# Optimization experiments

Measured on AMD Instinct MI355X. Metric: run time of the kernel, lower is better.

## Reference

```python
import jax, jax.numpy as jnp
import numpy as np

N_NODES = 20000
N_EDGES = 320000
IN_DIM = 64
H = 8      # num_heads
D = 16     # h_dim (out_dim)
CLAMP = 5.0


def setup_inputs() -> dict:
    key = jax.random.key(0)
    ks = jax.random.split(key, 12)
    inp = {
        'x': jax.random.normal(ks[0], (N_NODES, IN_DIM), jnp.float32),
        'edge_attr': jax.random.normal(ks[1], (N_EDGES, IN_DIM), jnp.float32),
        'edge_index': jax.random.randint(ks[2], (2, N_EDGES), 0, N_NODES),
        'Qw': jax.random.normal(ks[3], (IN_DIM, H * D), jnp.float32) * 0.1,
        'Qb': jnp.zeros((H * D,), jnp.float32),
        'Kw': jax.random.normal(ks[4], (IN_DIM, H * D), jnp.float32) * 0.1,
        'Kb': jnp.zeros((H * D,), jnp.float32),
        'Ew': jax.random.normal(ks[5], (IN_DIM, H * D * 2), jnp.float32) * 0.1,
        'Eb': jnp.zeros((H * D * 2,), jnp.float32),
        'Vw': jax.random.normal(ks[6], (IN_DIM, H * D), jnp.float32) * 0.1,
        'Vb': jnp.zeros((H * D,), jnp.float32),
        'Aw': jax.random.normal(ks[7], (D, H, 1), jnp.float32) * 0.1,
        'VeRow': jax.random.normal(ks[8], (D, H, D), jnp.float32) * 0.1,
    }
    return inp


def reference(x, edge_attr, edge_index, Qw, Qb, Kw, Kb, Ew, Eb, Vw, Vb, Aw, VeRow):
    N = x.shape[0]
    Ne = edge_attr.shape[0]
    src, dst = edge_index[0], edge_index[1]

    # node/edge projections (torch Linear stored as [in, out])
    Q_h = (x @ Qw + Qb).reshape(N, H, D)
    K_h = (x @ Kw + Kb).reshape(N, H, D)
    V_h = (x @ Vw + Vb).reshape(N, H, D)
    E = (edge_attr @ Ew + Eb).reshape(Ne, H, 2 * D)
    Ex1, Ex2 = E[:, :, :D], E[:, :, D:]

    # edge-wise additive score with signed-sqrt edge term  [Ne, H, D]
    s2 = Ex1 * Ex2
    score = K_h[src] + Q_h[dst] + jnp.sqrt(jax.nn.relu(s2)) - jnp.sqrt(jax.nn.relu(-s2))
    e_t = score
    oE = score.reshape(Ne, H * D)

    # attention logits: contract with Aw, clamp  [Ne, H, 1]
    a = jnp.einsum('ehd,dhc->ehc', score, Aw)
    a = jnp.clip(a, -CLAMP, CLAMP)

    # segment softmax over destination nodes
    m = jax.ops.segment_max(a, dst, num_segments=N)
    ea = jnp.exp(a - m[dst])
    denom = jax.ops.segment_sum(ea, dst, num_segments=N)
    attn = ea / (denom[dst] + 1e-16)  # [Ne, H, 1]

    # message passing: scatter-add to destination nodes
    oV = jax.ops.segment_sum(V_h[src] * attn, dst, num_segments=N)      # [N, H, D]
    rowV = jax.ops.segment_sum(e_t * attn, dst, num_segments=N)          # [N, H, D]
    rowV = jnp.einsum('nhd,dhc->nhc', rowV, VeRow)
    n_out = (oV + rowV).reshape(N, H * D)
    return n_out, oE
```

## Files before the change

kernel.cpp:

```cpp
#include <hip/hip_runtime.h>

#define IN_DIM 64
#define H 8
#define D 16
#define HD 128
#define CLAMP_V 5.0f
#define NCHUNK 8

typedef __attribute__((ext_vector_type(8))) short bf16x8;
typedef __attribute__((ext_vector_type(4))) float f32x4;

__device__ inline unsigned short f2b(float f) {
    unsigned int u = __float_as_uint(f);
    u += 0x7FFFu + ((u >> 16) & 1u);
    return (unsigned short)(u >> 16);
}
__device__ inline float b2f(unsigned short h) {
    return __uint_as_float((unsigned int)h << 16);
}
__device__ inline void split2(float f, unsigned short& hi, unsigned short& lo) {
    hi = f2b(f);
    lo = f2b(f - b2f(hi));
}

__global__ void __launch_bounds__(128) qkv_kernel(
    const float* __restrict__ x,
    const float* __restrict__ Qw, const float* __restrict__ Qb,
    const float* __restrict__ Kw, const float* __restrict__ Kb,
    const float* __restrict__ Vw, const float* __restrict__ Vb,
    float* __restrict__ Q, float* __restrict__ K, float* __restrict__ V)
{
    const int n0 = blockIdx.x * NCHUNK;
    const int t = threadIdx.x;
    __shared__ float xs[NCHUNK][IN_DIM];
    for (int i = t; i < NCHUNK * IN_DIM; i += 128)
        xs[i >> 6][i & 63] = x[(size_t)n0 * IN_DIM + i];
    __syncthreads();

    const float qb = Qb[t], kb = Kb[t], vb = Vb[t];
    float aq[NCHUNK], ak[NCHUNK], av[NCHUNK];
#pragma unroll
    for (int c = 0; c < NCHUNK; ++c) { aq[c] = qb; ak[c] = kb; av[c] = vb; }

#pragma unroll 4
    for (int k = 0; k < IN_DIM; ++k) {
        const float wq = Qw[k * HD + t];
        const float wk = Kw[k * HD + t];
        const float wv = Vw[k * HD + t];
#pragma unroll
        for (int c = 0; c < NCHUNK; ++c) {
            const float xv = xs[c][k];
            aq[c] = fmaf(xv, wq, aq[c]);
            ak[c] = fmaf(xv, wk, ak[c]);
            av[c] = fmaf(xv, wv, av[c]);
        }
    }
#pragma unroll
    for (int c = 0; c < NCHUNK; ++c) {
        Q[(size_t)(n0 + c) * HD + t] = aq[c];
        K[(size_t)(n0 + c) * HD + t] = ak[c];
        V[(size_t)(n0 + c) * HD + t] = av[c];
    }
}

__global__ void prep_ewt_kernel(const float* __restrict__ Ew, unsigned short* __restrict__ EwT)
{
    const int idx = blockIdx.x * 256 + threadIdx.x;
    const int k = idx >> 8, c = idx & 255;
    const float w = Ew[idx];
    unsigned short hi, lo;
    split2(w, hi, lo);
    EwT[c * 64 + k] = hi;
    EwT[16384 + c * 64 + k] = lo;
}

__global__ void zero_kernel(int* __restrict__ p, int n)
{
    const int i = blockIdx.x * blockDim.x + threadIdx.x;
    if (i < n) p[i] = 0;
}

__global__ void count_kernel(const int* __restrict__ ei, int* __restrict__ count, int Ne)
{
    const int e = blockIdx.x * blockDim.x + threadIdx.x;
    if (e < Ne) atomicAdd(&count[ei[Ne + e]], 1);
}

__global__ void __launch_bounds__(512) scan_block_kernel(
    const int* __restrict__ count, int* __restrict__ off_part, int* __restrict__ bsum, int N)
{
    __shared__ int buf[512];
    const int t = threadIdx.x;
    const int g = blockIdx.x * 512 + t;
    const int v = (g < N) ? count[g] : 0;
    buf[t] = v;
    __syncthreads();
    for (int s = 1; s < 512; s <<= 1) {
        const int add = (t >= s) ? buf[t - s] : 0;
        __syncthreads();
        buf[t] += add;
        __syncthreads();
    }
    if (g < N) off_part[g] = buf[t] - v;
    if (t == 511) bsum[blockIdx.x] = buf[511];
}

__global__ void __launch_bounds__(64) scan_tops_kernel(int* __restrict__ bsum, int NB)
{
    const int t = threadIdx.x;
    int v = (t < NB) ? bsum[t] : 0;
    const int orig = v;
#pragma unroll
    for (int s = 1; s < 64; s <<= 1) {
        const int o = __shfl_up(v, s);
        if (t >= s) v += o;
    }
    if (t < NB) bsum[t] = v - orig;
}

__global__ void __launch_bounds__(512) scan_add_kernel(
    const int* __restrict__ off_part, const int* __restrict__ bsum,
    int* __restrict__ off, int* __restrict__ cursor, int N)
{
    const int g = blockIdx.x * 512 + threadIdx.x;
    if (g < N) {
        const int o = off_part[g] + bsum[g >> 9];
        off[g] = o;
        cursor[g] = o;
    }
}

__global__ void scatter_kernel(const int* __restrict__ ei, int* __restrict__ cursor,
                               int* __restrict__ elist, int Ne)
{
    const int e = blockIdx.x * blockDim.x + threadIdx.x;
    if (e < Ne) {
        const int dst = ei[Ne + e];
        const int pos = atomicAdd(&cursor[dst], 1);
        elist[pos] = e;
    }
}

__global__ void __launch_bounds__(256) edge_kernel(
    const float* __restrict__ edge_attr, const int* __restrict__ ei,
    const unsigned short* __restrict__ EwTg,
    const float* __restrict__ Eb, const float* __restrict__ Aw,
    const float* __restrict__ Q, const float* __restrict__ K,
    float* __restrict__ oE, float* __restrict__ ea_ws, int Ne)
{
    const int t = threadIdx.x;
    const int e0 = blockIdx.x * 64;
    const int lane = t & 63, wid = t >> 6;
    const int m = lane & 15, q = lane >> 4;
    const int d = m;

    int sld[4], dld[4];
#pragma unroll
    for (int j = 0; j < 4; ++j) {
        const int el = wid * 16 + q * 4 + j;
        sld[j] = ei[e0 + el];
        dld[j] = ei[Ne + e0 + el];
    }

    const float* ar = edge_attr + (size_t)(e0 + wid * 16 + m) * 64 + q * 8;
    float av[16];
    *(float4*)(av)      = *(const float4*)(ar);
    *(float4*)(av + 4)  = *(const float4*)(ar + 4);
    *(float4*)(av + 8)  = *(const float4*)(ar + 32);
    *(float4*)(av + 12) = *(const float4*)(ar + 36);
    bf16x8 a0h, a0l, a1h, a1l;
#pragma unroll
    for (int i = 0; i < 8; ++i) {
        unsigned short hi, lo;
        split2(av[i], hi, lo);     a0h[i] = (short)hi; a0l[i] = (short)lo;
        split2(av[i + 8], hi, lo); a1h[i] = (short)hi; a1l[i] = (short)lo;
    }

#pragma unroll 2
    for (int h = 0; h < 8; ++h) {
        const int c1 = h * 32 + d;
        const int c2 = c1 + 16;
        const unsigned short* b1p = EwTg + c1 * 64 + q * 8;
        const unsigned short* b2p = EwTg + c2 * 64 + q * 8;
        const bf16x8 b00h = *(const bf16x8*)(b1p);
        const bf16x8 b01h = *(const bf16x8*)(b1p + 32);
        const bf16x8 b00l = *(const bf16x8*)(b1p + 16384);
        const bf16x8 b01l = *(const bf16x8*)(b1p + 16384 + 32);
        const bf16x8 b10h = *(const bf16x8*)(b2p);
        const bf16x8 b11h = *(const bf16x8*)(b2p + 32);
        const bf16x8 b10l = *(const bf16x8*)(b2p + 16384);
        const bf16x8 b11l = *(const bf16x8*)(b2p + 16384 + 32);

        f32x4 acc1 = {0.f, 0.f, 0.f, 0.f}, acc2 = {0.f, 0.f, 0.f, 0.f};
        acc1 = __builtin_amdgcn_mfma_f32_16x16x32_bf16(a0h, b00h, acc1, 0, 0, 0);
        acc1 = __builtin_amdgcn_mfma_f32_16x16x32_bf16(a1h, b01h, acc1, 0, 0, 0);
        acc1 = __builtin_amdgcn_mfma_f32_16x16x32_bf16(a0l, b00h, acc1, 0, 0, 0);
        acc1 = __builtin_amdgcn_mfma_f32_16x16x32_bf16(a1l, b01h, acc1, 0, 0, 0);
        acc1 = __builtin_amdgcn_mfma_f32_16x16x32_bf16(a0h, b00l, acc1, 0, 0, 0);
        acc1 = __builtin_amdgcn_mfma_f32_16x16x32_bf16(a1h, b01l, acc1, 0, 0, 0);
        acc2 = __builtin_amdgcn_mfma_f32_16x16x32_bf16(a0h, b10h, acc2, 0, 0, 0);
        acc2 = __builtin_amdgcn_mfma_f32_16x16x32_bf16(a1h, b11h, acc2, 0, 0, 0);
        acc2 = __builtin_amdgcn_mfma_f32_16x16x32_bf16(a0l, b10h, acc2, 0, 0, 0);
        acc2 = __builtin_amdgcn_mfma_f32_16x16x32_bf16(a1l, b11h, acc2, 0, 0, 0);
        acc2 = __builtin_amdgcn_mfma_f32_16x16x32_bf16(a0h, b10l, acc2, 0, 0, 0);
        acc2 = __builtin_amdgcn_mfma_f32_16x16x32_bf16(a1h, b11l, acc2, 0, 0, 0);

        const float eb1 = Eb[c1], eb2 = Eb[c2];
        const float aw = Aw[d * H + h];
        float eav[4];
#pragma unroll
        for (int j = 0; j < 4; ++j) {
            const int el = wid * 16 + q * 4 + j;
            const float x1 = acc1[j] + eb1;
            const float x2 = acc2[j] + eb2;
            const float s2 = x1 * x2;
            const float ss = copysignf(sqrtf(fabsf(s2)), s2);
            const float sc = K[(size_t)sld[j] * HD + h * D + d]
                           + Q[(size_t)dld[j] * HD + h * D + d] + ss;
            oE[(size_t)(e0 + el) * HD + h * D + d] = sc;
            float v = sc * aw;
            v += __shfl_xor(v, 1);
            v += __shfl_xor(v, 2);
            v += __shfl_xor(v, 4);
            v += __shfl_xor(v, 8);
            eav[j] = v;
        }
        if (d == 0) {
#pragma unroll
            for (int j = 0; j < 4; ++j) {
                const int el = wid * 16 + q * 4 + j;
                const float a = fminf(fmaxf(eav[j], -CLAMP_V), CLAMP_V);
                ea_ws[(size_t)(e0 + el) * H + h] = __expf(a - CLAMP_V);
            }
        }
    }
}

__global__ void __launch_bounds__(128) node_kernel(
    const int* __restrict__ ei, const int* __restrict__ off, const int* __restrict__ count,
    const int* __restrict__ elist,
    const float* __restrict__ V, const float* __restrict__ oE, const float* __restrict__ ea_ws,
    const float* __restrict__ VeRow,
    float* __restrict__ nout, int Ne)
{
    const int n = blockIdx.x;
    const int t = threadIdx.x;
    const int h = t >> 4;
    const int o = off[n], cnt = count[n];

    float accV = 0.0f, accE = 0.0f, den = 0.0f;
    int e_n = 0, s_n = 0;
    if (cnt > 0) { e_n = elist[o]; s_n = ei[e_n]; }
    for (int i = 0; i < cnt; ++i) {
        const int e = e_n, s = s_n;
        if (i + 1 < cnt) { e_n = elist[o + i + 1]; s_n = ei[e_n]; }
        const float w = ea_ws[(size_t)e * H + h];
        den += w;
        accV = fmaf(w, V[(size_t)s * HD + t], accV);
        accE = fmaf(w, oE[(size_t)e * HD + t], accE);
    }
    const float inv = 1.0f / (den + 1e-16f);
    accV *= inv;
    accE *= inv;

    __shared__ float sE[HD];
    sE[t] = accE;
    __syncthreads();

    float rowv = 0.0f;
    const int hb = h * D;
#pragma unroll
    for (int dp = 0; dp < D; ++dp)
        rowv = fmaf(sE[hb + dp], VeRow[dp * HD + t], rowv);

    nout[n * HD + t] = accV + rowv;
}

extern "C" void kernel_launch(void* const* d_in, const int* in_sizes, int n_in,
                              void* d_out, int out_size, void* d_ws, size_t ws_size,
                              hipStream_t stream)
{
    const float* x         = (const float*)d_in[0];
    const float* edge_attr = (const float*)d_in[1];
    const int*   ei        = (const int*)d_in[2];
    const float* Qw = (const float*)d_in[3];
    const float* Qb = (const float*)d_in[4];
    const float* Kw = (const float*)d_in[5];
    const float* Kb = (const float*)d_in[6];
    const float* Ew = (const float*)d_in[7];
    const float* Eb = (const float*)d_in[8];
    const float* Vw = (const float*)d_in[9];
    const float* Vb = (const float*)d_in[10];
    const float* Aw = (const float*)d_in[11];
    const float* VeRow = (const float*)d_in[12];

    const int N  = in_sizes[0] / IN_DIM;
    const int Ne = in_sizes[2] / 2;
    const int NB = (N + 511) / 512;

    char* ws = (char*)d_ws;
    float* Q       = (float*)ws; ws += (size_t)N * HD * 4;
    float* K       = (float*)ws; ws += (size_t)N * HD * 4;
    float* V       = (float*)ws; ws += (size_t)N * HD * 4;
    float* ea      = (float*)ws; ws += (size_t)Ne * H * 4;
    int*   count   = (int*)ws;   ws += (size_t)N * 4;
    int*   off     = (int*)ws;   ws += (size_t)N * 4;
    int*   cursor  = (int*)ws;   ws += (size_t)N * 4;
    int*   offp    = (int*)ws;   ws += (size_t)N * 4;
    int*   elist   = (int*)ws;   ws += (size_t)Ne * 4;
    int*   bsum    = (int*)ws;   ws += 256;
    unsigned short* EwT = (unsigned short*)ws; ws += 2 * 16384 * 2;

    float* nout = (float*)d_out;
    float* oE   = nout + (size_t)N * HD;

    hipLaunchKernelGGL(prep_ewt_kernel, dim3(64), dim3(256), 0, stream, Ew, EwT);
    hipLaunchKernelGGL(qkv_kernel, dim3(N / NCHUNK), dim3(128), 0, stream,
                       x, Qw, Qb, Kw, Kb, Vw, Vb, Q, K, V);
    hipLaunchKernelGGL(zero_kernel, dim3((N + 255) / 256), dim3(256), 0, stream, count, N);
    hipLaunchKernelGGL(count_kernel, dim3((Ne + 255) / 256), dim3(256), 0, stream, ei, count, Ne);
    hipLaunchKernelGGL(scan_block_kernel, dim3(NB), dim3(512), 0, stream, count, offp, bsum, N);
    hipLaunchKernelGGL(scan_tops_kernel, dim3(1), dim3(64), 0, stream, bsum, NB);
    hipLaunchKernelGGL(scan_add_kernel, dim3(NB), dim3(512), 0, stream, offp, bsum, off, cursor, N);
    hipLaunchKernelGGL(scatter_kernel, dim3((Ne + 255) / 256), dim3(256), 0, stream,
                       ei, cursor, elist, Ne);
    hipLaunchKernelGGL(edge_kernel, dim3(Ne / 64), dim3(256), 0, stream,
                       edge_attr, ei, EwT, Eb, Aw, Q, K, oE, ea, Ne);
    hipLaunchKernelGGL(node_kernel, dim3(N), dim3(128), 0, stream,
                       ei, off, count, elist, V, oE, ea, VeRow, nout, Ne);
}
```

Before: 582.0 us.

## Stage edge scores in LDS for coalesced stores and unroll node gather loop

The edge kernel now preloads all K/Q gathers for the eight heads up front, fully unrolls the head loop, and writes scores into a padded shared-memory tile. After a barrier it flushes that tile to oE with coalesced float4 stores instead of scattered 4-byte stores. The node kernel processes four incoming edges per iteration so more independent gather loads are in flight. The cost is roughly 33 KB of LDS per block and extra registers, which may lower occupancy.

After: 554.3 us. 4.8% less time.

```diff
diff --git a/kernel.cpp b/kernel.cpp
--- a/kernel.cpp
+++ b/kernel.cpp
@@ -141,6 +141,7 @@
     }
 }
 
+#define LSTR 132
 __global__ void __launch_bounds__(256) edge_kernel(
     const float* __restrict__ edge_attr, const int* __restrict__ ei,
     const unsigned short* __restrict__ EwTg,
@@ -148,11 +149,11 @@
     const float* __restrict__ Q, const float* __restrict__ K,
     float* __restrict__ oE, float* __restrict__ ea_ws, int Ne)
 {
+    __shared__ float soe[64 * LSTR];
     const int t = threadIdx.x;
     const int e0 = blockIdx.x * 64;
     const int lane = t & 63, wid = t >> 6;
     const int m = lane & 15, q = lane >> 4;
-    const int d = m;
 
     int sld[4], dld[4];
 #pragma unroll
@@ -168,6 +169,16 @@
     *(float4*)(av + 4)  = *(const float4*)(ar + 4);
     *(float4*)(av + 8)  = *(const float4*)(ar + 32);
     *(float4*)(av + 12) = *(const float4*)(ar + 36);
+
+    float kk[8][4], qq[8][4];
+#pragma unroll
+    for (int h = 0; h < 8; ++h)
+#pragma unroll
+        for (int j = 0; j < 4; ++j) {
+            kk[h][j] = K[(size_t)sld[j] * HD + h * D + m];
+            qq[h][j] = Q[(size_t)dld[j] * HD + h * D + m];
+        }
+
     bf16x8 a0h, a0l, a1h, a1l;
 #pragma unroll
     for (int i = 0; i < 8; ++i) {
@@ -176,9 +187,9 @@
         split2(av[i + 8], hi, lo); a1h[i] = (short)hi; a1l[i] = (short)lo;
     }
 
-#pragma unroll 2
+#pragma unroll
     for (int h = 0; h < 8; ++h) {
-        const int c1 = h * 32 + d;
+        const int c1 = h * 32 + m;
         const int c2 = c1 + 16;
         const unsigned short* b1p = EwTg + c1 * 64 + q * 8;
         const unsigned short* b2p = EwTg + c2 * 64 + q * 8;
@@ -206,7 +217,7 @@
         acc2 = __builtin_amdgcn_mfma_f32_16x16x32_bf16(a1h, b11l, acc2, 0, 0, 0);
 
         const float eb1 = Eb[c1], eb2 = Eb[c2];
-        const float aw = Aw[d * H + h];
+        const float aw = Aw[m * H + h];
         float eav[4];
 #pragma unroll
         for (int j = 0; j < 4; ++j) {
@@ -215,9 +226,8 @@
             const float x2 = acc2[j] + eb2;
             const float s2 = x1 * x2;
             const float ss = copysignf(sqrtf(fabsf(s2)), s2);
-            const float sc = K[(size_t)sld[j] * HD + h * D + d]
-                           + Q[(size_t)dld[j] * HD + h * D + d] + ss;
-            oE[(size_t)(e0 + el) * HD + h * D + d] = sc;
+            const float sc = kk[h][j] + qq[h][j] + ss;
+            soe[el * LSTR + h * D + m] = sc;
             float v = sc * aw;
             v += __shfl_xor(v, 1);
             v += __shfl_xor(v, 2);
@@ -225,7 +235,7 @@
             v += __shfl_xor(v, 8);
             eav[j] = v;
         }
-        if (d == 0) {
+        if (m == 0) {
 #pragma unroll
             for (int j = 0; j < 4; ++j) {
                 const int el = wid * 16 + q * 4 + j;
@@ -234,6 +244,15 @@
             }
         }
     }
+
+    __syncthreads();
+    float4* dst = (float4*)(oE + (size_t)e0 * HD);
+#pragma unroll
+    for (int u0 = 0; u0 < 2048; u0 += 256) {
+        const int u = u0 + t;
+        const int el = u >> 5, c4 = u & 31;
+        dst[u] = *(float4*)&soe[el * LSTR + c4 * 4];
+    }
 }
 
 __global__ void __launch_bounds__(128) node_kernel(
@@ -249,11 +268,32 @@
     const int o = off[n], cnt = count[n];
 
     float accV = 0.0f, accE = 0.0f, den = 0.0f;
-    int e_n = 0, s_n = 0;
-    if (cnt > 0) { e_n = elist[o]; s_n = ei[e_n]; }
-    for (int i = 0; i < cnt; ++i) {
-        const int e = e_n, s = s_n;
-        if (i + 1 < cnt) { e_n = elist[o + i + 1]; s_n = ei[e_n]; }
+    int i = 0;
+    for (; i + 4 <= cnt; i += 4) {
+        const int e0_ = elist[o + i],     e1_ = elist[o + i + 1];
+        const int e2_ = elist[o + i + 2], e3_ = elist[o + i + 3];
+        const int s0_ = ei[e0_], s1_ = ei[e1_], s2_ = ei[e2_], s3_ = ei[e3_];
+        const float w0 = ea_ws[(size_t)e0_ * H + h];
+        const float w1 = ea_ws[(size_t)e1_ * H + h];
+        const float w2 = ea_ws[(size_t)e2_ * H + h];
+        const float w3 = ea_ws[(size_t)e3_ * H + h];
+        const float v0 = V[(size_t)s0_ * HD + t];
+        const float v1 = V[(size_t)s1_ * HD + t];
+        const float v2 = V[(size_t)s2_ * HD + t];
+        const float v3 = V[(size_t)s3_ * HD + t];
+        const float p0 = oE[(size_t)e0_ * HD + t];
+        const float p1 = oE[(size_t)e1_ * HD + t];
+        const float p2 = oE[(size_t)e2_ * HD + t];
+        const float p3 = oE[(size_t)e3_ * HD + t];
+        den += (w0 + w1) + (w2 + w3);
+        accV = fmaf(w0, v0, accV); accV = fmaf(w1, v1, accV);
+        accV = fmaf(w2, v2, accV); accV = fmaf(w3, v3, accV);
+        accE = fmaf(w0, p0, accE); accE = fmaf(w1, p1, accE);
+        accE = fmaf(w2, p2, accE); accE = fmaf(w3, p3, accE);
+    }
+    for (; i < cnt; ++i) {
+        const int e = elist[o + i];
+        const int s = ei[e];
         const float w = ea_ws[(size_t)e * H + h];
         den += w;
         accV = fmaf(w, V[(size_t)s * HD + t], accV);
```
